# Kernel tuning notes

Hardware: AMD Instinct MI355X
Metric: run time of the kernel (lower is better)

The kernel has to match this reference:

```python
import jax, jax.numpy as jnp
import numpy as np

C = 1024
EPS = 1e-5


def _layernorm(y, gamma, beta):
    mu = jnp.mean(y, axis=-1, keepdims=True)
    var = jnp.mean(jnp.square(y - mu), axis=-1, keepdims=True)
    return (y - mu) * jax.lax.rsqrt(var + EPS) * gamma + beta


def setup_inputs() -> dict:
    key = jax.random.key(0)
    ks = jax.random.split(key, 8)
    B, T = 32, 1024
    s = 1.0 / np.sqrt(2 * C)
    x = jax.random.normal(ks[0], (B, T, C), dtype=jnp.float32)
    Wa = jax.random.uniform(ks[1], (2 * C, 2 * C), jnp.float32, -s, s)
    ba = jax.random.uniform(ks[2], (2 * C,), jnp.float32, -s, s)
    Wb = jax.random.uniform(ks[3], (C, 2 * C), jnp.float32, -s, s)
    bb = jax.random.uniform(ks[4], (C,), jnp.float32, -s, s)
    gamma = jnp.ones((C,), jnp.float32)
    beta = jnp.zeros((C,), jnp.float32)
    return {"x": x, "Wa": Wa, "ba": ba, "Wb": Wb, "bb": bb, "gamma": gamma, "beta": beta}


def reference(x, Wa, ba, Wb, bb, gamma, beta):
    B, T, Cc = x.shape

    def step(h, x_t):
        # h: (B, C), x_t: (B, C)
        z = jnp.concatenate([h, x_t], axis=-1)              # (B, 2C)
        y = jax.nn.gelu(z @ Wa.T + ba, approximate=False)   # (B, 2C)
        y = y @ Wb.T + bb                                    # (B, C)
        h_new = _layernorm(y, gamma, beta) + y               # norm(y) + y
        return h_new, h_new

    h0 = jnp.zeros((B, Cc), dtype=x.dtype)
    _, hs = jax.lax.scan(step, h0, jnp.swapaxes(x, 0, 1))   # (T, B, C)
    return jnp.swapaxes(hs, 0, 1)                            # (B, T, C)
```

## Files before the change

kernel.cpp:

```cpp
#include <hip/hip_runtime.h>
#include <math.h>

#define CC    1024
#define CC2   2048
#define BB    32
#define TT    1024
#define NBLK  256
#define NTHR  512
#define LNEPS 1e-5f

#define WS_Y    32768
#define WS_Y2   98304
#define WS_BARF 131072

#define RB0   0
#define RB1   16448
#define RWOFF 8224
#define SC0F  32896
#define GB_G  35200
#define GB_B  36224
#define SMEMN 37248

#define AUX_CACHED 0
#define AUX_COH    17

typedef float    nfloat4 __attribute__((ext_vector_type(4)));
typedef unsigned nuint4  __attribute__((ext_vector_type(4)));

#define WAIT_VM(N)  do { asm volatile("s_waitcnt vmcnt(" #N ")" ::: "memory"); \
                         __builtin_amdgcn_sched_barrier(0); } while (0)
#define WAIT_LGKM0  do { asm volatile("s_waitcnt lgkmcnt(0)" ::: "memory"); \
                         __builtin_amdgcn_sched_barrier(0); } while (0)
#define SBAR()      do { __builtin_amdgcn_s_barrier(); \
                         __builtin_amdgcn_sched_barrier(0); } while (0)

__global__ void rpe_init(float* __restrict__ ws) {
    unsigned* bar = (unsigned*)(ws + WS_BARF);
    const int i = blockIdx.x * blockDim.x + threadIdx.x;
    if (i < 512) bar[i] = 0u;
}

__device__ __forceinline__ unsigned spin_load_u32(const unsigned* p) {
    unsigned v;
    asm volatile("global_load_dword %0, %1, off sc0 sc1\n\ts_waitcnt vmcnt(0)"
                 : "=&v"(v) : "v"(p) : "memory");
    return v;
}
__device__ __forceinline__ nuint4 coh_load_u32x4(const unsigned* p) {
    nuint4 v;
    asm volatile("global_load_dwordx4 %0, %1, off sc0 sc1\n\ts_waitcnt vmcnt(0)"
                 : "=&v"(v) : "v"(p) : "memory");
    return v;
}
__device__ __forceinline__ nfloat4 coh_load_f32x4_nowait(const float* p) {
    nfloat4 v;
    asm volatile("global_load_dwordx4 %0, %1, off sc0 sc1"
                 : "=&v"(v) : "v"(p));
    return v;
}
__device__ __forceinline__ void async_cp16(const float* g, float* l) {
    __builtin_amdgcn_global_load_lds(
        (const __attribute__((address_space(1))) void*)g,
        (__attribute__((address_space(3))) void*)l, 16, 0, AUX_CACHED);
}
__device__ __forceinline__ void async_cp16_coh(const float* g, float* l) {
    __builtin_amdgcn_global_load_lds(
        (const __attribute__((address_space(1))) void*)g,
        (__attribute__((address_space(3))) void*)l, 16, 0, AUX_COH);
}
__device__ __forceinline__ void coh_store(float* p, float v) {
    __hip_atomic_store(p, v, __ATOMIC_RELAXED, __HIP_MEMORY_SCOPE_AGENT);
}
__device__ __forceinline__ void coh_store_u32(unsigned* p, unsigned v) {
    __hip_atomic_store(p, v, __ATOMIC_RELAXED, __HIP_MEMORY_SCOPE_AGENT);
}
__device__ __forceinline__ float gelu_exact(float a) {
    return 0.5f * a * (1.0f + erff(a * 0.70710678118654752440f));
}

__device__ __forceinline__ void bar_arrive(unsigned* arr, unsigned phase,
                                           int blk, int tid) {
    __threadfence_block();
    __syncthreads();
    if (tid == 0) coh_store_u32(&arr[blk], phase);
}
__device__ __forceinline__ void bar_wait(unsigned* arr, unsigned* gen,
                                         unsigned phase, int blk, int tid) {
    if (blk == 0) {
        if (tid < 64) {
            unsigned* a4 = arr + (tid << 2);
            int n = 0;
            for (;;) {
                nuint4 v;
                if ((n & 7) == 7) {
                    v[0] = __hip_atomic_fetch_add(&a4[0], 0u, __ATOMIC_RELAXED, __HIP_MEMORY_SCOPE_AGENT);
                    v[1] = __hip_atomic_fetch_add(&a4[1], 0u, __ATOMIC_RELAXED, __HIP_MEMORY_SCOPE_AGENT);
                    v[2] = __hip_atomic_fetch_add(&a4[2], 0u, __ATOMIC_RELAXED, __HIP_MEMORY_SCOPE_AGENT);
                    v[3] = __hip_atomic_fetch_add(&a4[3], 0u, __ATOMIC_RELAXED, __HIP_MEMORY_SCOPE_AGENT);
                } else {
                    v = coh_load_u32x4(a4);
                }
                ++n;
                unsigned m0 = v[0] < v[1] ? v[0] : v[1];
                unsigned m1 = v[2] < v[3] ? v[2] : v[3];
                unsigned m  = m0 < m1 ? m0 : m1;
                if (__ballot(m >= phase) == ~0ull) break;
                __builtin_amdgcn_s_sleep(1);
            }
            if (tid == 0) coh_store_u32(gen, phase);
        }
    } else if (tid == 0) {
        int n = 0;
        for (;;) {
            unsigned g = ((n & 7) == 7)
                ? __hip_atomic_fetch_add(gen, 0u, __ATOMIC_RELAXED, __HIP_MEMORY_SCOPE_AGENT)
                : spin_load_u32(gen);
            ++n;
            if (g >= phase) break;
            __builtin_amdgcn_s_sleep(2);
        }
    }
    SBAR();
}

extern "C" __global__ void __launch_bounds__(NTHR)
rpe_main(const float* __restrict__ x,  const float* __restrict__ Wa,
         const float* __restrict__ ba, const float* __restrict__ Wb,
         const float* __restrict__ bbv, const float* __restrict__ gamma,
         const float* __restrict__ beta, float* __restrict__ out,
         float* __restrict__ ws)
{
    float*    y_ws  = ws + WS_Y;
    float*    y2_ws = ws + WS_Y2;
    unsigned* arr   = (unsigned*)(ws + WS_BARF);
    unsigned* gen   = arr + 320;

    const int tid  = threadIdx.x;
    const int blk  = blockIdx.x;
    const int wv   = tid >> 6;
    const int lane = tid & 63;
    const int pos  = lane & 7;
    const int ks   = lane >> 3;

    __shared__ float smem[SMEMN];

    const int xcd  = blk & 7;
    const int slot = blk >> 3;

    const int j0  = (xcd * 16 + (slot & 15)) * 16;
    const int b0A = (slot >> 4) * 16;
    const int i0  = (xcd * 8 + (slot & 7)) * 16;
    const int b0B = (slot >> 3) * 8;

    const int jtA = pos & 1;
    const int btA = pos >> 1;
    const int ipB = pos & 3;
    const int bpB = pos >> 2;

    const int  lr     = slot & 15;
    const bool writer = ((slot & 7) == xcd) && (wv == (lr >> 1));
    const int  rrW    = lr & 1;

    for (int i = tid; i < CC; i += NTHR) {
        smem[GB_G + i] = gamma[i];
        smem[GB_B + i] = beta[i];
    }

    float ba_reg = (tid < 256) ? ba[j0 + (tid & 15)] : 0.f;
    float bb_reg = (tid < 128) ? bbv[i0 + (tid & 15)] : 0.f;
    asm volatile("" : "+v"(ba_reg), "+v"(bb_reg));

    int t;
    nfloat4 hz[8];
    float acc[32];
    float accB[16];

    auto issue_wa = [&](int c, int base) {
        #pragma unroll
        for (int s = 0; s < 4; ++s) {
            const int q = wv * 4 + s;
            const int jr = q >> 1, hf = q & 1;
            async_cp16(Wa + (size_t)(j0 + jr) * CC2 + c * 512 + hf * 256 + lane * 4,
                       &smem[base + RWOFF + jr * 512 + (jr >= 8 ? 4 : 0) + hf * 256]);
        }
    };
    auto issue_x = [&](int c, int base) {
        #pragma unroll
        for (int s = 0; s < 4; ++s) {
            const int q = wv * 4 + s;
            const int r = q >> 1, hf = q & 1;
            async_cp16(x + (size_t)(b0A + r) * TT * CC + (size_t)t * CC
                         + (c - 2) * 512 + hf * 256 + lane * 4,
                       &smem[base + r * 512 + ((r >> 2) << 2) + hf * 256]);
        }
    };
    auto dsw_z = [&](int c, int base) {
        #pragma unroll
        for (int s = 0; s < 4; ++s) {
            const int r = wv * 2 + (s >> 1), hf = s & 1;
            *(nfloat4*)&smem[base + r * 512 + ((r >> 2) << 2) + hf * 256 + lane * 4]
                = hz[c * 4 + s];
        }
    };
    auto issue_y = [&](int c, int base) {
        #pragma unroll
        for (int s = 0; s < 2; ++s) {
            const int q = wv * 2 + s;
            const int r = q >> 1, hf = q & 1;
            async_cp16_coh(y_ws + (size_t)(b0B + r) * CC2 + c * 512 + hf * 256 + lane * 4,
                           &smem[base + r * 512 + ((r >> 2) << 2) + hf * 256]);
        }
    };
    auto issue_wb = [&](int c, int base) {
        #pragma unroll
        for (int s = 0; s < 4; ++s) {
            const int q = wv * 4 + s;
            const int ir = q >> 1, hf = q & 1;
            async_cp16(Wb + (size_t)(i0 + ir) * CC2 + c * 512 + hf * 256 + lane * 4,
                       &smem[base + RWOFF + ir * 512 + ((ir >> 2) << 2) + hf * 256]);
        }
    };
    auto computeA = [&](int base) {
        const int zb = base, wb = base + RWOFF;
        const int k0 = (wv * 8 + ks) * 8;
        #pragma unroll
        for (int kk = 0; kk < 8; kk += 4) {
            const int k = k0 + kk;
            float4 zz[4];
            #pragma unroll
            for (int b2 = 0; b2 < 4; ++b2)
                zz[b2] = *(const float4*)&smem[zb + (btA * 4 + b2) * 512 + btA * 4 + k];
            #pragma unroll
            for (int jj = 0; jj < 8; ++jj) {
                const float4 ww = *(const float4*)&smem[wb + (jtA * 8 + jj) * 512 + jtA * 4 + k];
                #pragma unroll
                for (int b2 = 0; b2 < 4; ++b2) {
                    const float4 zv = zz[b2];
                    float& A = acc[jj * 4 + b2];
                    A = fmaf(ww.x, zv.x, fmaf(ww.y, zv.y, fmaf(ww.z, zv.z, fmaf(ww.w, zv.w, A))));
                }
            }
        }
    };
    auto computeB = [&](int base) {
        const int yb = base, wb = base + RWOFF;
        const int k0 = (wv * 8 + ks) * 8;
        #pragma unroll
        for (int kk = 0; kk < 8; kk += 4) {
            const int k = k0 + kk;
            float4 yy[4];
            #pragma unroll
            for (int b2 = 0; b2 < 4; ++b2)
                yy[b2] = *(const float4*)&smem[yb + (bpB * 4 + b2) * 512 + bpB * 4 + k];
            #pragma unroll
            for (int ii = 0; ii < 4; ++ii) {
                const float4 ww = *(const float4*)&smem[wb + (ipB * 4 + ii) * 512 + ipB * 4 + k];
                #pragma unroll
                for (int b2 = 0; b2 < 4; ++b2) {
                    const float4 yv = yy[b2];
                    float& A = accB[ii * 4 + b2];
                    A = fmaf(ww.x, yv.x, fmaf(ww.y, yv.y, fmaf(ww.z, yv.z, fmaf(ww.w, yv.w, A))));
                }
            }
        }
    };

    unsigned ph = 0;

    issue_wa(0, RB0);
    issue_wa(1, RB1);

    for (t = 0; t <= TT; ++t) {
        if (t > 0) {
            #pragma unroll
            for (int u = 0; u < 8; ++u) {
                const int c2 = u >> 2, rr = (u >> 1) & 1, hf = u & 1;
                hz[u] = coh_load_f32x4_nowait(
                    y2_ws + (size_t)(b0A + wv * 2 + rr) * CC + c2 * 512 + hf * 256 + lane * 4);
            }
        }
        WAIT_VM(0);
        if (t > 0) {
            float s0 = 0.f, ss0 = 0.f, s1 = 0.f, ss1 = 0.f;
            #pragma unroll
            for (int u = 0; u < 8; ++u) {
                const int rr = (u >> 1) & 1;
                const float ls  = hz[u][0] + hz[u][1] + hz[u][2] + hz[u][3];
                const float lss = hz[u][0]*hz[u][0] + hz[u][1]*hz[u][1]
                                + hz[u][2]*hz[u][2] + hz[u][3]*hz[u][3];
                if (rr == 0) { s0 += ls; ss0 += lss; } else { s1 += ls; ss1 += lss; }
            }
            #pragma unroll
            for (int off = 1; off < 64; off <<= 1) {
                s0  += __shfl_xor(s0,  off);
                ss0 += __shfl_xor(ss0, off);
                s1  += __shfl_xor(s1,  off);
                ss1 += __shfl_xor(ss1, off);
            }
            const float mu0 = s0 * (1.0f / CC);
            const float mu1 = s1 * (1.0f / CC);
            const float rs0 = 1.0f / sqrtf(ss0 * (1.0f / CC) - mu0 * mu0 + LNEPS);
            const float rs1 = 1.0f / sqrtf(ss1 * (1.0f / CC) - mu1 * mu1 + LNEPS);
            #pragma unroll
            for (int u = 0; u < 8; ++u) {
                const int rr  = (u >> 1) & 1;
                const int col = (u >> 2) * 512 + (u & 1) * 256 + lane * 4;
                const nfloat4 g4 = *(const nfloat4*)&smem[GB_G + col];
                const nfloat4 b4 = *(const nfloat4*)&smem[GB_B + col];
                const float mu = rr ? mu1 : mu0;
                const float rs = rr ? rs1 : rs0;
                #pragma unroll
                for (int e = 0; e < 4; ++e)
                    hz[u][e] = (hz[u][e] - mu) * rs * g4[e] + b4[e] + hz[u][e];
            }
            if (writer) {
                #pragma unroll
                for (int c2 = 0; c2 < 2; ++c2)
                #pragma unroll
                for (int hf = 0; hf < 2; ++hf) {
                    const int u = c2 * 4 + rrW * 2 + hf;
                    __builtin_nontemporal_store(hz[u],
                        (nfloat4*)(out + ((size_t)(b0A + lr) * TT + (t - 1)) * CC
                                       + c2 * 512 + hf * 256 + lane * 4));
                }
            }
        } else {
            const nfloat4 z4 = {0.f, 0.f, 0.f, 0.f};
            #pragma unroll
            for (int u = 0; u < 8; ++u) hz[u] = z4;
        }
        if (t == TT) break;

        #pragma unroll
        for (int a = 0; a < 32; ++a) acc[a] = 0.f;

        dsw_z(0, RB0); WAIT_LGKM0; SBAR();
        computeA(RB0);
        SBAR();
        dsw_z(1, RB1); issue_x(2, RB0); issue_wa(2, RB0); WAIT_LGKM0; SBAR();
        computeA(RB1);
        SBAR();
        issue_x(3, RB1); issue_wa(3, RB1); WAIT_VM(8); SBAR();
        computeA(RB0);
        WAIT_VM(0); SBAR();
        computeA(RB1);

        #pragma unroll
        for (int a = 0; a < 32; ++a) {
            float v = acc[a];
            v += __shfl_xor(v, 8);
            v += __shfl_xor(v, 16);
            v += __shfl_xor(v, 32);
            acc[a] = v;
        }
        if (lane < 8) {
            #pragma unroll
            for (int a4 = 0; a4 < 32; a4 += 4)
                *(float4*)&smem[SC0F + wv * 288 + lane * 36 + a4] =
                    make_float4(acc[a4], acc[a4 + 1], acc[a4 + 2], acc[a4 + 3]);
        }
        WAIT_LGKM0; SBAR();
        if (tid < 256) {
            const int bl = tid >> 4, jl = tid & 15;
            const int p2 = (bl >> 2) * 2 + (jl >> 3);
            const int a2 = (jl & 7) * 4 + (bl & 3);
            float s = ba_reg;
            #pragma unroll
            for (int w2 = 0; w2 < 8; ++w2) s += smem[SC0F + w2 * 288 + p2 * 36 + a2];
            coh_store(&y_ws[(size_t)(b0A + bl) * CC2 + j0 + jl], gelu_exact(s));
        }
        {
            const unsigned p1 = ++ph;
            bar_arrive(arr, p1, blk, tid);
            issue_wb(0, RB0);
            issue_wb(1, RB1);
            bar_wait(arr, gen, p1, blk, tid);
        }

        #pragma unroll
        for (int a = 0; a < 16; ++a) accB[a] = 0.f;

        issue_y(0, RB0); issue_y(1, RB1);
        WAIT_VM(2); SBAR();
        computeB(RB0);
        SBAR();
        issue_wb(2, RB0); issue_y(2, RB0); WAIT_VM(6); SBAR();
        computeB(RB1);
        SBAR();
        issue_wb(3, RB1); issue_y(3, RB1); WAIT_VM(6); SBAR();
        computeB(RB0);
        WAIT_VM(0); SBAR();
        computeB(RB1);

        #pragma unroll
        for (int a = 0; a < 16; ++a) {
            float v = accB[a];
            v += __shfl_xor(v, 8);
            v += __shfl_xor(v, 16);
            v += __shfl_xor(v, 32);
            accB[a] = v;
        }
        if (lane < 8) {
            #pragma unroll
            for (int a4 = 0; a4 < 16; a4 += 4)
                *(float4*)&smem[SC0F + wv * 160 + lane * 20 + a4] =
                    make_float4(accB[a4], accB[a4 + 1], accB[a4 + 2], accB[a4 + 3]);
        }
        WAIT_LGKM0; SBAR();
        if (tid < 128) {
            const int bl = tid >> 4, il = tid & 15;
            const int p2 = (bl >> 2) * 4 + (il >> 2);
            const int a2 = (il & 3) * 4 + (bl & 3);
            float s = bb_reg;
            #pragma unroll
            for (int w2 = 0; w2 < 8; ++w2) s += smem[SC0F + w2 * 160 + p2 * 20 + a2];
            coh_store(&y2_ws[(size_t)(b0B + bl) * CC + i0 + il], s);
        }
        {
            const unsigned p2g = ++ph;
            bar_arrive(arr, p2g, blk, tid);
            issue_wa(0, RB0);
            issue_wa(1, RB1);
            bar_wait(arr, gen, p2g, blk, tid);
        }
    }
}

extern "C" void kernel_launch(void* const* d_in, const int* in_sizes, int n_in,
                              void* d_out, int out_size, void* d_ws, size_t ws_size,
                              hipStream_t stream) {
    const float* x     = (const float*)d_in[0];
    const float* Wa    = (const float*)d_in[1];
    const float* ba    = (const float*)d_in[2];
    const float* Wb    = (const float*)d_in[3];
    const float* bb    = (const float*)d_in[4];
    const float* gamma = (const float*)d_in[5];
    const float* beta  = (const float*)d_in[6];
    float* out = (float*)d_out;
    float* ws  = (float*)d_ws;

    hipLaunchKernelGGL(rpe_init, dim3(1), dim3(512), 0, stream, ws);
    hipLaunchKernelGGL(rpe_main, dim3(NBLK), dim3(NTHR), 0, stream,
                       x, Wa, ba, Wb, bb, gamma, beta, out, ws);
}
```

Measured before the change: 29.75 ms.

## Replace master-gathered grid barrier with distributed atomic counters and reorder phase-A prefetch

Replaces the two-level grid barrier, where block 0 polls 256 per-block flags and then publishes a generation word, with 64 atomic counters. Each block increments one counter and every block polls all 64 counters directly, which removes the extra gen-flag hop. Phase A is also reordered so the x/Wa chunks that do not depend on h (indices 2,3) are prefetched before the barrier, and the h-dependent chunks are computed after. This is meant to cut barrier latency on each of the 2048 grid syncs and to overlap loads with waiting, at the cost of more atomic contention and all blocks polling global memory.

```diff
diff --git a/kernel.cpp b/kernel.cpp
--- a/kernel.cpp
+++ b/kernel.cpp
@@ -37,7 +37,7 @@
 __global__ void rpe_init(float* __restrict__ ws) {
     unsigned* bar = (unsigned*)(ws + WS_BARF);
     const int i = blockIdx.x * blockDim.x + threadIdx.x;
-    if (i < 512) bar[i] = 0u;
+    if (i < 128) bar[i] = 0u;
 }
 
 __device__ __forceinline__ unsigned spin_load_u32(const unsigned* p) {
@@ -46,12 +46,6 @@
                  : "=&v"(v) : "v"(p) : "memory");
     return v;
 }
-__device__ __forceinline__ nuint4 coh_load_u32x4(const unsigned* p) {
-    nuint4 v;
-    asm volatile("global_load_dwordx4 %0, %1, off sc0 sc1\n\ts_waitcnt vmcnt(0)"
-                 : "=&v"(v) : "v"(p) : "memory");
-    return v;
-}
 __device__ __forceinline__ nfloat4 coh_load_f32x4_nowait(const float* p) {
     nfloat4 v;
     asm volatile("global_load_dwordx4 %0, %1, off sc0 sc1"
@@ -71,53 +65,26 @@
 __device__ __forceinline__ void coh_store(float* p, float v) {
     __hip_atomic_store(p, v, __ATOMIC_RELAXED, __HIP_MEMORY_SCOPE_AGENT);
 }
-__device__ __forceinline__ void coh_store_u32(unsigned* p, unsigned v) {
-    __hip_atomic_store(p, v, __ATOMIC_RELAXED, __HIP_MEMORY_SCOPE_AGENT);
-}
 __device__ __forceinline__ float gelu_exact(float a) {
     return 0.5f * a * (1.0f + erff(a * 0.70710678118654752440f));
 }
 
-__device__ __forceinline__ void bar_arrive(unsigned* arr, unsigned phase,
-                                           int blk, int tid) {
-    __threadfence_block();
-    __syncthreads();
-    if (tid == 0) coh_store_u32(&arr[blk], phase);
-}
-__device__ __forceinline__ void bar_wait(unsigned* arr, unsigned* gen,
-                                         unsigned phase, int blk, int tid) {
-    if (blk == 0) {
-        if (tid < 64) {
-            unsigned* a4 = arr + (tid << 2);
-            int n = 0;
-            for (;;) {
-                nuint4 v;
-                if ((n & 7) == 7) {
-                    v[0] = __hip_atomic_fetch_add(&a4[0], 0u, __ATOMIC_RELAXED, __HIP_MEMORY_SCOPE_AGENT);
-                    v[1] = __hip_atomic_fetch_add(&a4[1], 0u, __ATOMIC_RELAXED, __HIP_MEMORY_SCOPE_AGENT);
-                    v[2] = __hip_atomic_fetch_add(&a4[2], 0u, __ATOMIC_RELAXED, __HIP_MEMORY_SCOPE_AGENT);
-                    v[3] = __hip_atomic_fetch_add(&a4[3], 0u, __ATOMIC_RELAXED, __HIP_MEMORY_SCOPE_AGENT);
-                } else {
-                    v = coh_load_u32x4(a4);
-                }
-                ++n;
-                unsigned m0 = v[0] < v[1] ? v[0] : v[1];
-                unsigned m1 = v[2] < v[3] ? v[2] : v[3];
-                unsigned m  = m0 < m1 ? m0 : m1;
-                if (__ballot(m >= phase) == ~0ull) break;
-                __builtin_amdgcn_s_sleep(1);
-            }
-            if (tid == 0) coh_store_u32(gen, phase);
-        }
-    } else if (tid == 0) {
+__device__ __forceinline__ void bar_core(unsigned* cnt, unsigned phase,
+                                         int blk, int tid) {
+    if (tid == 0)
+        __hip_atomic_fetch_add(&cnt[blk & 63], 1u,
+                               __ATOMIC_RELAXED, __HIP_MEMORY_SCOPE_AGENT);
+    if (tid < 64) {
+        const unsigned target = 4u * phase;
+        unsigned* w = cnt + tid;
         int n = 0;
         for (;;) {
-            unsigned g = ((n & 7) == 7)
-                ? __hip_atomic_fetch_add(gen, 0u, __ATOMIC_RELAXED, __HIP_MEMORY_SCOPE_AGENT)
-                : spin_load_u32(gen);
-            ++n;
-            if (g >= phase) break;
-            __builtin_amdgcn_s_sleep(2);
+            unsigned v = ((++n & 1023) == 0)
+                ? __hip_atomic_fetch_add(w, 0u, __ATOMIC_RELAXED,
+                                         __HIP_MEMORY_SCOPE_AGENT)
+                : spin_load_u32(w);
+            if (__ballot(v >= target) == ~0ull) break;
+            __builtin_amdgcn_s_sleep(1);
         }
     }
     SBAR();
@@ -132,8 +99,7 @@
 {
     float*    y_ws  = ws + WS_Y;
     float*    y2_ws = ws + WS_Y2;
-    unsigned* arr   = (unsigned*)(ws + WS_BARF);
-    unsigned* gen   = arr + 320;
+    unsigned* cnt   = (unsigned*)(ws + WS_BARF);
 
     const int tid  = threadIdx.x;
     const int blk  = blockIdx.x;
@@ -267,20 +233,22 @@
 
     unsigned ph = 0;
 
-    issue_wa(0, RB0);
-    issue_wa(1, RB1);
-
     for (t = 0; t <= TT; ++t) {
         if (t > 0) {
+            __threadfence_block();
+            __syncthreads();
+            if (t < TT) {
+                issue_x(2, RB0); issue_x(3, RB1);
+                issue_wa(2, RB0); issue_wa(3, RB1);
+            }
+            bar_core(cnt, ++ph, blk, tid);
             #pragma unroll
             for (int u = 0; u < 8; ++u) {
                 const int c2 = u >> 2, rr = (u >> 1) & 1, hf = u & 1;
                 hz[u] = coh_load_f32x4_nowait(
                     y2_ws + (size_t)(b0A + wv * 2 + rr) * CC + c2 * 512 + hf * 256 + lane * 4);
             }
-        }
-        WAIT_VM(0);
-        if (t > 0) {
+            WAIT_VM(0);
             float s0 = 0.f, ss0 = 0.f, s1 = 0.f, ss1 = 0.f;
             #pragma unroll
             for (int u = 0; u < 8; ++u) {
@@ -325,22 +293,26 @@
                 }
             }
         } else {
+            issue_x(2, RB0); issue_x(3, RB1);
+            issue_wa(2, RB0); issue_wa(3, RB1);
             const nfloat4 z4 = {0.f, 0.f, 0.f, 0.f};
             #pragma unroll
             for (int u = 0; u < 8; ++u) hz[u] = z4;
+            WAIT_VM(0);
         }
         if (t == TT) break;
 
         #pragma unroll
         for (int a = 0; a < 32; ++a) acc[a] = 0.f;
 
-        dsw_z(0, RB0); WAIT_LGKM0; SBAR();
+        SBAR();
         computeA(RB0);
         SBAR();
-        dsw_z(1, RB1); issue_x(2, RB0); issue_wa(2, RB0); WAIT_LGKM0; SBAR();
+        dsw_z(0, RB0); issue_wa(0, RB0);
         computeA(RB1);
         SBAR();
-        issue_x(3, RB1); issue_wa(3, RB1); WAIT_VM(8); SBAR();
+        dsw_z(1, RB1); issue_wa(1, RB1);
+        WAIT_VM(4); WAIT_LGKM0; SBAR();
         computeA(RB0);
         WAIT_VM(0); SBAR();
         computeA(RB1);
@@ -369,13 +341,11 @@
             for (int w2 = 0; w2 < 8; ++w2) s += smem[SC0F + w2 * 288 + p2 * 36 + a2];
             coh_store(&y_ws[(size_t)(b0A + bl) * CC2 + j0 + jl], gelu_exact(s));
         }
-        {
-            const unsigned p1 = ++ph;
-            bar_arrive(arr, p1, blk, tid);
-            issue_wb(0, RB0);
-            issue_wb(1, RB1);
-            bar_wait(arr, gen, p1, blk, tid);
-        }
+
+        __threadfence_block();
+        __syncthreads();
+        issue_wb(0, RB0); issue_wb(1, RB1);
+        bar_core(cnt, ++ph, blk, tid);
 
         #pragma unroll
         for (int a = 0; a < 16; ++a) accB[a] = 0.f;
@@ -384,10 +354,12 @@
         WAIT_VM(2); SBAR();
         computeB(RB0);
         SBAR();
-        issue_wb(2, RB0); issue_y(2, RB0); WAIT_VM(6); SBAR();
+        issue_wb(2, RB0); issue_y(2, RB0);
+        WAIT_VM(6); SBAR();
         computeB(RB1);
         SBAR();
-        issue_wb(3, RB1); issue_y(3, RB1); WAIT_VM(6); SBAR();
+        issue_wb(3, RB1); issue_y(3, RB1);
+        WAIT_VM(6); SBAR();
         computeB(RB0);
         WAIT_VM(0); SBAR();
         computeB(RB1);
@@ -415,13 +387,6 @@
             #pragma unroll
             for (int w2 = 0; w2 < 8; ++w2) s += smem[SC0F + w2 * 160 + p2 * 20 + a2];
             coh_store(&y2_ws[(size_t)(b0B + bl) * CC + i0 + il], s);
-        }
-        {
-            const unsigned p2g = ++ph;
-            bar_arrive(arr, p2g, blk, tid);
-            issue_wa(0, RB0);
-            issue_wa(1, RB1);
-            bar_wait(arr, gen, p2g, blk, tid);
         }
     }
 }
```

New measurement: 43.10 ms. +44.9%, slower.
